# Performance work log

Hardware: AMD Instinct MI355X
Metric: run time of the kernel (lower is better)

## Reference

```python
import jax, jax.numpy as jnp
import numpy as np

B, DIM, H, W = 16, 512, 32, 32
N_CB, VOCAB, D_CB = 8, 1024, 64  # DIM == N_CB * D_CB


def setup_inputs() -> dict:
    key = jax.random.key(0)
    k1, k2 = jax.random.split(key)
    z = jax.random.normal(k1, (B, DIM, H, W), dtype=jnp.float32)
    codebooks = jax.random.normal(k2, (N_CB, VOCAB, D_CB), dtype=jnp.float32) * 0.02
    return {"z": z, "codebooks": codebooks}


def reference(z, codebooks):
    # Eval-mode forward of the multi-codebook (residual-style) VQ:
    # per-codebook squared-distance argmin, gather, straight-through, commitment loss.
    b, d, h, w = z.shape
    n_cb, vocab, d_cb = codebooks.shape
    # rearrange 'b d h w -> (b h w) d', then chunk d into n_cb contiguous parts
    z_flat = z.transpose(0, 2, 3, 1).reshape(-1, n_cb, d_cb)  # (N, n_cb, d_cb)
    # ||z||^2 - 2 z.c + ||c||^2  -> (N, n_cb, vocab)
    dists = (
        jnp.sum(z_flat * z_flat, axis=-1, keepdims=True)
        - 2.0 * jnp.einsum("ncd,cvd->ncv", z_flat, codebooks)
        + jnp.sum(codebooks * codebooks, axis=-1)[None, :, :]
    )
    idx = jnp.argmin(dists, axis=-1)  # (N, n_cb) int
    # gather per-codebook nearest embedding
    q = codebooks[jnp.arange(n_cb)[None, :], idx]  # (N, n_cb, d_cb)
    # commitment: mean over all elements (equal-size chunks => same as per-chunk mse averaged)
    commitment = jnp.mean((z_flat - jax.lax.stop_gradient(q)) ** 2)
    # straight-through estimator
    q_st = z_flat + jax.lax.stop_gradient(q - z_flat)
    quantized = q_st.reshape(b, h, w, d).transpose(0, 3, 1, 2)  # (B, D, H, W)
    indices = idx.reshape(b, h, w, n_cb).transpose(0, 3, 1, 2)  # (B, n_cb, H, W)
    return quantized, indices, commitment
```

## Files before the change

kernel.cpp:

```cpp
#include <hip/hip_runtime.h>
#include <float.h>

#define DIM   512
#define HW    1024
#define NCB   8
#define VOC   1024
#define DCB   64

#define THREADS   256
#define POS_TILE  128
#define VCHUNK    128
#define NCHUNK    8
#define CAP       16
#define MARGIN    0.012f

#define Q_ELEMS   8388608
#define I_ELEMS   131072
#define C_OFFSET  8519680

#define WS_CC_OFF 256
#define WS_CB_OFF 33024

typedef __attribute__((ext_vector_type(8))) short          short8;
typedef __attribute__((ext_vector_type(8))) unsigned short ushort8;
typedef __attribute__((ext_vector_type(4))) float          floatx4;

__device__ __forceinline__ unsigned short f2bf(float f) {
    unsigned u = __builtin_bit_cast(unsigned, f);
    unsigned r = u + 0x7FFFu + ((u >> 16) & 1u);
    return (unsigned short)(r >> 16);
}

__global__ __launch_bounds__(128) void vq_prep_kernel(const float* __restrict__ cbk,
                                                      char* __restrict__ ws,
                                                      float* __restrict__ cc,
                                                      unsigned short* __restrict__ cbkBf) {
#pragma clang fp contract(off)
    int t = blockIdx.x * 128 + threadIdx.x;
    if (t == 0) { ((float*)ws)[0] = 0.f; ((unsigned*)ws)[1] = 0u; }
    const float4* row = (const float4*)(cbk + (long)t * DCB);
    float c[64];
#pragma unroll
    for (int i = 0; i < 16; ++i) {
        float4 v = row[i];
        c[i * 4 + 0] = v.x; c[i * 4 + 1] = v.y;
        c[i * 4 + 2] = v.z; c[i * 4 + 3] = v.w;
    }
    float r[8];
#pragma unroll
    for (int j = 0; j < 8; ++j) { float sq = c[j] * c[j]; r[j] = sq; }
#pragma unroll
    for (int i = 1; i < 8; ++i)
#pragma unroll
        for (int j = 0; j < 8; ++j) { float sq = c[i * 8 + j] * c[i * 8 + j]; r[j] = r[j] + sq; }
    cc[t] = ((r[0] + r[1]) + (r[2] + r[3])) + ((r[4] + r[5]) + (r[6] + r[7]));
    const int swz = (t & 7) << 3;
#pragma unroll
    for (int g8 = 0; g8 < 8; ++g8) {
        ushort8 w;
#pragma unroll
        for (int e = 0; e < 8; ++e) w[e] = f2bf(-2.0f * c[g8 * 8 + e]);
        *(ushort8*)&cbkBf[(long)t * 64 + ((g8 * 8) ^ swz)] = w;
    }
}

struct SmemT {
    unsigned short zsb[POS_TILE * DCB];
    unsigned short csb[2][VCHUNK * DCB];
    float          ccS[VOC];
    unsigned       candI[POS_TILE * CAP];
    unsigned       cnt[POS_TILE];
    unsigned       idxF[POS_TILE];
    float          wred[4];
};

__device__ __forceinline__ void stage_cb(unsigned short* ldsDst,
                                         const unsigned short* gSrc,
                                         int wid, int lane) {
#pragma unroll
    for (int i = 0; i < 4; ++i) {
        const int off = wid * 2048 + i * 512;
        const unsigned short* g = gSrc + off + lane * 8;
        unsigned short* l = ldsDst + off;
        __builtin_amdgcn_global_load_lds(
            (const __attribute__((address_space(1))) unsigned int*)(const void*)g,
            (__attribute__((address_space(3))) unsigned int*)(void*)l,
            16, 0, 0);
    }
}

__device__ __forceinline__ float np_dist_stream(const float* zcol, const float4* cr,
                                                float zz, float ccv) {
#pragma clang fp contract(off)
    float p[16];
#pragma unroll
    for (int l = 0; l < 16; ++l) p[l] = 0.f;
#pragma unroll
    for (int j = 0; j < 4; ++j) {
        float4 c0 = cr[j * 4 + 0], c1 = cr[j * 4 + 1];
        float4 c2 = cr[j * 4 + 2], c3 = cr[j * 4 + 3];
        float cl[16] = {c0.x, c0.y, c0.z, c0.w, c1.x, c1.y, c1.z, c1.w,
                        c2.x, c2.y, c2.z, c2.w, c3.x, c3.y, c3.z, c3.w};
#pragma unroll
        for (int l = 0; l < 16; ++l)
            p[l] = __builtin_fmaf(zcol[(long)(j * 16 + l) * POS_TILE], cl[l], p[l]);
    }
    float s8[8], s4[4];
#pragma unroll
    for (int l = 0; l < 8; ++l) s8[l] = p[l] + p[l + 8];
#pragma unroll
    for (int l = 0; l < 4; ++l) s4[l] = s8[l] + s8[l + 4];
    float u0 = s4[0] + s4[2];
    float u1 = s4[1] + s4[3];
    float E  = u0 + u1;
    float t  = zz - 2.0f * E;
    return t + ccv;
}

__global__ __launch_bounds__(THREADS, 2) void vq_main_kernel(
    const float* __restrict__ z, const float* __restrict__ cbk,
    const float* __restrict__ ccTab, const unsigned short* __restrict__ cbkBf,
    float* __restrict__ commitWs, unsigned* __restrict__ doneCnt,
    float* __restrict__ out)
{
    __shared__ SmemT sm;

    const int tid   = threadIdx.x;
    const int lane  = tid & 63;
    const int wid   = tid >> 6;
    const int l15   = lane & 15;
    const int lg    = lane >> 4;
    const int wpos0 = wid * 32;
    const int cb    = blockIdx.x & 7;
    const int tile  = blockIdx.x >> 3;
    const int b     = tile >> 3;
    const int hw0   = (tile & 7) * POS_TILE;

    const long zBase  = (long)b * (DIM * HW) + (long)cb * DCB * HW + hw0;
    const long cbBase = (long)cb * (VOC * DCB);
    const unsigned short* cbkBfCb = cbkBf + cbBase;

    stage_cb(sm.csb[0], cbkBfCb, wid, lane);

    for (int i = 0; i < 16; ++i) {
        int e   = i * THREADS + tid;
        int kp  = e >> 7;
        int pos = e & 127;
        int k   = kp * 2;
        float v0 = z[zBase + (long)k * HW + pos];
        float v1 = z[zBase + (long)(k + 1) * HW + pos];
        unsigned pack = (unsigned)f2bf(v0) | ((unsigned)f2bf(v1) << 16);
        *(unsigned*)&sm.zsb[pos * 64 + (k ^ ((pos & 7) << 3))] = pack;
    }
    ((float4*)sm.ccS)[tid] = ((const float4*)(ccTab + cb * VOC))[tid];
    if (tid < POS_TILE) sm.cnt[tid] = 0;
    __syncthreads();

    float runBest[2] = {FLT_MAX, FLT_MAX};
    int cur = 0;

    for (int chunk = 0; chunk < NCHUNK; ++chunk) {
        if (chunk < 7)
            stage_cb(sm.csb[cur ^ 1], cbkBfCb + (long)(chunk + 1) * VCHUNK * DCB, wid, lane);

        const unsigned short* cs = sm.csb[cur];

        floatx4 acc[8][2];
#pragma unroll
        for (int ct = 0; ct < 8; ++ct) {
            float4 ci = *(const float4*)&sm.ccS[chunk * VCHUNK + ct * 16 + lg * 4];
            floatx4 a = {ci.x, ci.y, ci.z, ci.w};
            acc[ct][0] = a; acc[ct][1] = a;
        }

#pragma unroll
        for (int ks = 0; ks < 2; ++ks) {
            short8 bz[2];
#pragma unroll
            for (int pt = 0; pt < 2; ++pt) {
                int row = wpos0 + pt * 16 + l15;
                bz[pt] = *(const short8*)&sm.zsb[row * 64 + ((ks * 32 + lg * 8) ^ ((row & 7) << 3))];
            }
#pragma unroll
            for (int ct = 0; ct < 8; ++ct) {
                int crow = ct * 16 + l15;
                short8 ac = *(const short8*)&cs[crow * 64 + ((ks * 32 + lg * 8) ^ ((crow & 7) << 3))];
#pragma unroll
                for (int pt = 0; pt < 2; ++pt)
                    acc[ct][pt] = __builtin_amdgcn_mfma_f32_16x16x32_bf16(ac, bz[pt], acc[ct][pt], 0, 0, 0);
            }
        }

#pragma unroll
        for (int pt = 0; pt < 2; ++pt) {
            float m = acc[0][pt][0];
#pragma unroll
            for (int ct = 0; ct < 8; ++ct)
#pragma unroll
                for (int r = 0; r < 4; ++r) m = fminf(m, acc[ct][pt][r]);
            m = fminf(m, __shfl_xor(m, 16, 64));
            m = fminf(m, __shfl_xor(m, 32, 64));
            runBest[pt] = fminf(runBest[pt], m);
            const float thr = runBest[pt] + MARGIN;
            const int pos = wpos0 + pt * 16 + l15;
#pragma unroll
            for (int ct = 0; ct < 8; ++ct)
#pragma unroll
                for (int r = 0; r < 4; ++r) {
                    if (acc[ct][pt][r] <= thr) {
                        unsigned idx  = chunk * VCHUNK + ct * 16 + lg * 4 + r;
                        unsigned slot = atomicAdd(&sm.cnt[pos], 1u);
                        if (slot < CAP) sm.candI[pos * CAP + slot] = idx;
                    }
                }
        }
        __syncthreads();
        cur ^= 1;
    }

    float* zf32 = (float*)sm.csb;
#pragma unroll
    for (int i = 0; i < 8; ++i) {
        int e4   = i * THREADS + tid;
        int k    = e4 >> 5;
        int posq = e4 & 31;
        float4 v = *(const float4*)(z + zBase + (long)k * HW + posq * 4);
        *(float4*)&zf32[k * POS_TILE + posq * 4] = v;
    }
    __syncthreads();

    if (tid < POS_TILE) {
        const int pos = tid;
        const float* zcol = zf32 + pos;
        float zz;
        {
#pragma clang fp contract(off)
            float r[8];
#pragma unroll
            for (int j = 0; j < 8; ++j) { float v = zcol[(long)j * POS_TILE]; r[j] = v * v; }
#pragma unroll
            for (int i = 1; i < 8; ++i)
#pragma unroll
                for (int j = 0; j < 8; ++j) {
                    float v = zcol[(long)(i * 8 + j) * POS_TILE];
                    r[j] = r[j] + v * v;
                }
            zz = ((r[0] + r[1]) + (r[2] + r[3])) + ((r[4] + r[5]) + (r[6] + r[7]));
        }
        const unsigned n = sm.cnt[pos];
        float bd = FLT_MAX; unsigned bi = 0xFFFFFFFFu;
        if (n <= CAP) {
            for (unsigned s = 0; s < n; ++s) {
                unsigned vi = sm.candI[pos * CAP + s];
                float d = np_dist_stream(zcol, (const float4*)(cbk + cbBase + (long)vi * DCB),
                                         zz, sm.ccS[vi]);
                if (d < bd || (d == bd && vi < bi)) { bd = d; bi = vi; }
            }
        } else {
            for (unsigned vi = 0; vi < VOC; ++vi) {
                float d = np_dist_stream(zcol, (const float4*)(cbk + cbBase + (long)vi * DCB),
                                         zz, sm.ccS[vi]);
                if (d < bd) { bd = d; bi = vi; }
            }
        }
        sm.idxF[pos] = bi;
        out[Q_ELEMS + (long)b * (NCB * HW) + cb * HW + hw0 + pos] = (float)bi;
    }
    __syncthreads();

    {
        const int pos   = tid & 127;
        const int khalf = tid >> 7;
        const unsigned vi = sm.idxF[pos];
        const float* crow = cbk + cbBase + (long)vi * DCB + khalf * 32;
        const float* zcol = zf32 + pos + khalf * 32 * POS_TILE;
        float* qp = out + (long)b * (DIM * HW) + (long)(cb * DCB + khalf * 32) * HW + hw0 + pos;
        float csum = 0.f;
#pragma unroll
        for (int j4 = 0; j4 < 8; ++j4) {
            float4 cv = *(const float4*)(crow + j4 * 4);
            float z0 = zcol[(j4 * 4 + 0) * POS_TILE];
            float z1 = zcol[(j4 * 4 + 1) * POS_TILE];
            float z2 = zcol[(j4 * 4 + 2) * POS_TILE];
            float z3 = zcol[(j4 * 4 + 3) * POS_TILE];
            qp[(long)(j4 * 4 + 0) * HW] = (cv.x - z0) + z0;
            qp[(long)(j4 * 4 + 1) * HW] = (cv.y - z1) + z1;
            qp[(long)(j4 * 4 + 2) * HW] = (cv.z - z2) + z2;
            qp[(long)(j4 * 4 + 3) * HW] = (cv.w - z3) + z3;
            float d0 = z0 - cv.x; csum = fmaf(d0, d0, csum);
            float d1 = z1 - cv.y; csum = fmaf(d1, d1, csum);
            float d2 = z2 - cv.z; csum = fmaf(d2, d2, csum);
            float d3 = z3 - cv.w; csum = fmaf(d3, d3, csum);
        }
#pragma unroll
        for (int m = 1; m < 64; m <<= 1) csum += __shfl_xor(csum, m, 64);
        if (lane == 0) sm.wred[wid] = csum;
    }
    __syncthreads();

    if (tid == 0) {
        atomicAdd(commitWs, sm.wred[0] + sm.wred[1] + sm.wred[2] + sm.wred[3]);
        __threadfence();
        unsigned d = atomicAdd(doneCnt, 1u);
        if (d == 1023u) {
            __threadfence();
            float tot = atomicAdd(commitWs, 0.0f);
            out[C_OFFSET] = tot * (1.0f / 8388608.0f);
        }
    }
}

extern "C" void kernel_launch(void* const* d_in, const int* in_sizes, int n_in,
                              void* d_out, int out_size, void* d_ws, size_t ws_size,
                              hipStream_t stream) {
    (void)in_sizes; (void)n_in; (void)out_size; (void)ws_size;
    const float* z   = (const float*)d_in[0];
    const float* cbk = (const float*)d_in[1];
    float* out = (float*)d_out;
    char*  ws  = (char*)d_ws;
    float*          commitWs = (float*)ws;
    unsigned*       doneCnt  = (unsigned*)(ws + 4);
    float*          ccTab    = (float*)(ws + WS_CC_OFF);
    unsigned short* cbkBf    = (unsigned short*)(ws + WS_CB_OFF);

    vq_prep_kernel<<<dim3(64), dim3(128), 0, stream>>>(cbk, ws, ccTab, cbkBf);
    vq_main_kernel<<<dim3(1024), dim3(THREADS), 0, stream>>>(z, cbk, ccTab, cbkBf,
                                                             commitWs, doneCnt, out);
}
```

Measured before the change: 193.4 us.

## Pre-swizzle codebook into MFMA fragment layout and read directly from global

The prep kernel now writes the bf16 codebook already arranged in per-lane MFMA operand order, so the main kernel loads A fragments straight from global/L2 instead of double-buffering chunks through LDS with barriers. The z fragments are held in registers for all chunks, the fp32 z tile and cc table are no longer staged in LDS, and the rescoring and quantize steps run per wave from global memory with a shuffle instead of block barriers. The smaller LDS footprint allows a launch bound of four blocks per SM, and the commitment sum is spread over 64 atomic slots. The cost is more global/L2 traffic and latency per MFMA operand load, with no LDS reuse across waves.

```diff
diff --git a/kernel.cpp b/kernel.cpp
--- a/kernel.cpp
+++ b/kernel.cpp
@@ -18,8 +18,10 @@
 #define I_ELEMS   131072
 #define C_OFFSET  8519680
 
-#define WS_CC_OFF 256
-#define WS_CB_OFF 33024
+#define WS_DONE_OFF   0
+#define WS_SLOT_OFF   256
+#define WS_CC_OFF     1024
+#define WS_CB_OFF     33792
 
 typedef __attribute__((ext_vector_type(8))) short          short8;
 typedef __attribute__((ext_vector_type(8))) unsigned short ushort8;
@@ -31,66 +33,64 @@
     return (unsigned short)(r >> 16);
 }
 
-__global__ __launch_bounds__(128) void vq_prep_kernel(const float* __restrict__ cbk,
-                                                      char* __restrict__ ws,
+__global__ __launch_bounds__(256) void vq_prep_kernel(const float* __restrict__ cbk,
+                                                      unsigned* __restrict__ doneCnt,
+                                                      float* __restrict__ slots,
                                                       float* __restrict__ cc,
                                                       unsigned short* __restrict__ cbkBf) {
 #pragma clang fp contract(off)
-    int t = blockIdx.x * 128 + threadIdx.x;
-    if (t == 0) { ((float*)ws)[0] = 0.f; ((unsigned*)ws)[1] = 0u; }
-    const float4* row = (const float4*)(cbk + (long)t * DCB);
-    float c[64];
-#pragma unroll
+    __shared__ float zr[256 * 65];
+    const int tid   = threadIdx.x;
+    const int rows0 = blockIdx.x * 256;
+
+    if (blockIdx.x == 0 && tid < 65) {
+        if (tid == 0) *doneCnt = 0u;
+        else slots[tid - 1] = 0.f;
+    }
+
     for (int i = 0; i < 16; ++i) {
-        float4 v = row[i];
-        c[i * 4 + 0] = v.x; c[i * 4 + 1] = v.y;
-        c[i * 4 + 2] = v.z; c[i * 4 + 3] = v.w;
-    }
-    float r[8];
-#pragma unroll
-    for (int j = 0; j < 8; ++j) { float sq = c[j] * c[j]; r[j] = sq; }
-#pragma unroll
-    for (int i = 1; i < 8; ++i)
-#pragma unroll
-        for (int j = 0; j < 8; ++j) { float sq = c[i * 8 + j] * c[i * 8 + j]; r[j] = r[j] + sq; }
-    cc[t] = ((r[0] + r[1]) + (r[2] + r[3])) + ((r[4] + r[5]) + (r[6] + r[7]));
-    const int swz = (t & 7) << 3;
-#pragma unroll
-    for (int g8 = 0; g8 < 8; ++g8) {
+        int e4  = i * 256 + tid;
+        int row = e4 >> 4;
+        int k4  = (e4 & 15) * 4;
+        float4 v = ((const float4*)cbk)[(long)rows0 * 16 + e4];
+        zr[row * 65 + k4 + 0] = v.x;
+        zr[row * 65 + k4 + 1] = v.y;
+        zr[row * 65 + k4 + 2] = v.z;
+        zr[row * 65 + k4 + 3] = v.w;
+    }
+    __syncthreads();
+
+    {
+        const float* c = &zr[tid * 65];
+        float r[8];
+#pragma unroll
+        for (int j = 0; j < 8; ++j) { float v = c[j]; r[j] = v * v; }
+#pragma unroll
+        for (int i = 1; i < 8; ++i)
+#pragma unroll
+            for (int j = 0; j < 8; ++j) { float v = c[i * 8 + j]; r[j] = r[j] + v * v; }
+        cc[rows0 + tid] = ((r[0] + r[1]) + (r[2] + r[3])) + ((r[4] + r[5]) + (r[6] + r[7]));
+    }
+
+#pragma unroll
+    for (int it = 0; it < 8; ++it) {
+        int row = it * 32 + (tid >> 3);
+        int g8  = tid & 7;
         ushort8 w;
 #pragma unroll
-        for (int e = 0; e < 8; ++e) w[e] = f2bf(-2.0f * c[g8 * 8 + e]);
-        *(ushort8*)&cbkBf[(long)t * 64 + ((g8 * 8) ^ swz)] = w;
-    }
-}
-
-struct SmemT {
-    unsigned short zsb[POS_TILE * DCB];
-    unsigned short csb[2][VCHUNK * DCB];
-    float          ccS[VOC];
-    unsigned       candI[POS_TILE * CAP];
-    unsigned       cnt[POS_TILE];
-    unsigned       idxF[POS_TILE];
-    float          wred[4];
-};
-
-__device__ __forceinline__ void stage_cb(unsigned short* ldsDst,
-                                         const unsigned short* gSrc,
-                                         int wid, int lane) {
-#pragma unroll
-    for (int i = 0; i < 4; ++i) {
-        const int off = wid * 2048 + i * 512;
-        const unsigned short* g = gSrc + off + lane * 8;
-        unsigned short* l = ldsDst + off;
-        __builtin_amdgcn_global_load_lds(
-            (const __attribute__((address_space(1))) unsigned int*)(const void*)g,
-            (__attribute__((address_space(3))) unsigned int*)(void*)l,
-            16, 0, 0);
-    }
-}
-
-__device__ __forceinline__ float np_dist_stream(const float* zcol, const float4* cr,
-                                                float zz, float ccv) {
+        for (int e = 0; e < 8; ++e) w[e] = f2bf(-2.0f * zr[row * 65 + g8 * 8 + e]);
+        int g     = rows0 + row;
+        int code  = g & 1023;
+        int chunk = code >> 7, ct = (code >> 4) & 7, l15 = code & 15;
+        int ks    = g8 >> 2,  lg = g8 & 3;
+        long dst = (long)(g >> 10) * 65536 +
+                   ((((chunk * 8 + ct) * 2 + ks) * 64) + lg * 16 + l15) * 8;
+        *(ushort8*)&cbkBf[dst] = w;
+    }
+}
+
+__device__ __forceinline__ float np_dist_g(const float* zp, const float4* cr,
+                                           float zz, float ccv) {
 #pragma clang fp contract(off)
     float p[16];
 #pragma unroll
@@ -103,7 +103,7 @@
                         c2.x, c2.y, c2.z, c2.w, c3.x, c3.y, c3.z, c3.w};
 #pragma unroll
         for (int l = 0; l < 16; ++l)
-            p[l] = __builtin_fmaf(zcol[(long)(j * 16 + l) * POS_TILE], cl[l], p[l]);
+            p[l] = __builtin_fmaf(zp[(long)(j * 16 + l) * HW], cl[l], p[l]);
     }
     float s8[8], s4[4];
 #pragma unroll
@@ -117,10 +117,16 @@
     return t + ccv;
 }
 
-__global__ __launch_bounds__(THREADS, 2) void vq_main_kernel(
+struct SmemT {
+    unsigned short zsb[POS_TILE * DCB];
+    unsigned       candI[POS_TILE * CAP];
+    unsigned       cnt[POS_TILE];
+};
+
+__global__ __launch_bounds__(THREADS, 4) void vq_main_kernel(
     const float* __restrict__ z, const float* __restrict__ cbk,
     const float* __restrict__ ccTab, const unsigned short* __restrict__ cbkBf,
-    float* __restrict__ commitWs, unsigned* __restrict__ doneCnt,
+    float* __restrict__ slots, unsigned* __restrict__ doneCnt,
     float* __restrict__ out)
 {
     __shared__ SmemT sm;
@@ -138,9 +144,8 @@
 
     const long zBase  = (long)b * (DIM * HW) + (long)cb * DCB * HW + hw0;
     const long cbBase = (long)cb * (VOC * DCB);
-    const unsigned short* cbkBfCb = cbkBf + cbBase;
-
-    stage_cb(sm.csb[0], cbkBfCb, wid, lane);
+    const unsigned short* cbA  = cbkBf + (long)cb * 65536;
+    const float*          ccRow = ccTab + cb * VOC;
 
     for (int i = 0; i < 16; ++i) {
         int e   = i * THREADS + tid;
@@ -152,44 +157,37 @@
         unsigned pack = (unsigned)f2bf(v0) | ((unsigned)f2bf(v1) << 16);
         *(unsigned*)&sm.zsb[pos * 64 + (k ^ ((pos & 7) << 3))] = pack;
     }
-    ((float4*)sm.ccS)[tid] = ((const float4*)(ccTab + cb * VOC))[tid];
     if (tid < POS_TILE) sm.cnt[tid] = 0;
     __syncthreads();
 
+    short8 bz[2][2];
+#pragma unroll
+    for (int pt = 0; pt < 2; ++pt)
+#pragma unroll
+        for (int ks = 0; ks < 2; ++ks) {
+            int row = wpos0 + pt * 16 + l15;
+            bz[pt][ks] = *(const short8*)&sm.zsb[row * 64 + ((ks * 32 + lg * 8) ^ ((row & 7) << 3))];
+        }
+
     float runBest[2] = {FLT_MAX, FLT_MAX};
-    int cur = 0;
 
     for (int chunk = 0; chunk < NCHUNK; ++chunk) {
-        if (chunk < 7)
-            stage_cb(sm.csb[cur ^ 1], cbkBfCb + (long)(chunk + 1) * VCHUNK * DCB, wid, lane);
-
-        const unsigned short* cs = sm.csb[cur];
-
         floatx4 acc[8][2];
 #pragma unroll
         for (int ct = 0; ct < 8; ++ct) {
-            float4 ci = *(const float4*)&sm.ccS[chunk * VCHUNK + ct * 16 + lg * 4];
+            float4 ci = *(const float4*)&ccRow[chunk * VCHUNK + ct * 16 + lg * 4];
             floatx4 a = {ci.x, ci.y, ci.z, ci.w};
             acc[ct][0] = a; acc[ct][1] = a;
         }
-
-#pragma unroll
-        for (int ks = 0; ks < 2; ++ks) {
-            short8 bz[2];
-#pragma unroll
-            for (int pt = 0; pt < 2; ++pt) {
-                int row = wpos0 + pt * 16 + l15;
-                bz[pt] = *(const short8*)&sm.zsb[row * 64 + ((ks * 32 + lg * 8) ^ ((row & 7) << 3))];
+#pragma unroll
+        for (int ks = 0; ks < 2; ++ks)
+#pragma unroll
+            for (int ct = 0; ct < 8; ++ct) {
+                short8 ac = *(const short8*)&cbA[((((chunk * 8 + ct) * 2 + ks) << 6) + lane) << 3];
+#pragma unroll
+                for (int pt = 0; pt < 2; ++pt)
+                    acc[ct][pt] = __builtin_amdgcn_mfma_f32_16x16x32_bf16(ac, bz[pt][ks], acc[ct][pt], 0, 0, 0);
             }
-#pragma unroll
-            for (int ct = 0; ct < 8; ++ct) {
-                int crow = ct * 16 + l15;
-                short8 ac = *(const short8*)&cs[crow * 64 + ((ks * 32 + lg * 8) ^ ((crow & 7) << 3))];
-#pragma unroll
-                for (int pt = 0; pt < 2; ++pt)
-                    acc[ct][pt] = __builtin_amdgcn_mfma_f32_16x16x32_bf16(ac, bz[pt], acc[ct][pt], 0, 0, 0);
-            }
-        }
 
 #pragma unroll
         for (int pt = 0; pt < 2; ++pt) {
@@ -214,75 +212,62 @@
                     }
                 }
         }
-        __syncthreads();
-        cur ^= 1;
-    }
-
-    float* zf32 = (float*)sm.csb;
-#pragma unroll
-    for (int i = 0; i < 8; ++i) {
-        int e4   = i * THREADS + tid;
-        int k    = e4 >> 5;
-        int posq = e4 & 31;
-        float4 v = *(const float4*)(z + zBase + (long)k * HW + posq * 4);
-        *(float4*)&zf32[k * POS_TILE + posq * 4] = v;
-    }
-    __syncthreads();
-
-    if (tid < POS_TILE) {
-        const int pos = tid;
-        const float* zcol = zf32 + pos;
+    }
+
+    unsigned bi = 0xFFFFFFFFu;
+    if (lane < 32) {
+        const int pos = wpos0 + lane;
+        const float* zp = z + zBase + pos;
         float zz;
         {
 #pragma clang fp contract(off)
             float r[8];
 #pragma unroll
-            for (int j = 0; j < 8; ++j) { float v = zcol[(long)j * POS_TILE]; r[j] = v * v; }
+            for (int j = 0; j < 8; ++j) { float v = zp[(long)j * HW]; r[j] = v * v; }
 #pragma unroll
             for (int i = 1; i < 8; ++i)
 #pragma unroll
                 for (int j = 0; j < 8; ++j) {
-                    float v = zcol[(long)(i * 8 + j) * POS_TILE];
+                    float v = zp[(long)(i * 8 + j) * HW];
                     r[j] = r[j] + v * v;
                 }
             zz = ((r[0] + r[1]) + (r[2] + r[3])) + ((r[4] + r[5]) + (r[6] + r[7]));
         }
         const unsigned n = sm.cnt[pos];
-        float bd = FLT_MAX; unsigned bi = 0xFFFFFFFFu;
+        float bd = FLT_MAX;
         if (n <= CAP) {
             for (unsigned s = 0; s < n; ++s) {
                 unsigned vi = sm.candI[pos * CAP + s];
-                float d = np_dist_stream(zcol, (const float4*)(cbk + cbBase + (long)vi * DCB),
-                                         zz, sm.ccS[vi]);
+                float d = np_dist_g(zp, (const float4*)(cbk + cbBase + (long)vi * DCB),
+                                    zz, ccRow[vi]);
                 if (d < bd || (d == bd && vi < bi)) { bd = d; bi = vi; }
             }
         } else {
             for (unsigned vi = 0; vi < VOC; ++vi) {
-                float d = np_dist_stream(zcol, (const float4*)(cbk + cbBase + (long)vi * DCB),
-                                         zz, sm.ccS[vi]);
+                float d = np_dist_g(zp, (const float4*)(cbk + cbBase + (long)vi * DCB),
+                                    zz, ccRow[vi]);
                 if (d < bd) { bd = d; bi = vi; }
             }
         }
-        sm.idxF[pos] = bi;
         out[Q_ELEMS + (long)b * (NCB * HW) + cb * HW + hw0 + pos] = (float)bi;
     }
-    __syncthreads();
-
+
+    const unsigned vi = (unsigned)__shfl((int)bi, lane & 31, 64);
     {
-        const int pos   = tid & 127;
-        const int khalf = tid >> 7;
-        const unsigned vi = sm.idxF[pos];
+        const int posl  = lane & 31;
+        const int pos   = wpos0 + posl;
+        const int khalf = lane >> 5;
         const float* crow = cbk + cbBase + (long)vi * DCB + khalf * 32;
-        const float* zcol = zf32 + pos + khalf * 32 * POS_TILE;
+        const float* zp   = z + zBase + pos + (long)khalf * 32 * HW;
         float* qp = out + (long)b * (DIM * HW) + (long)(cb * DCB + khalf * 32) * HW + hw0 + pos;
         float csum = 0.f;
 #pragma unroll
         for (int j4 = 0; j4 < 8; ++j4) {
             float4 cv = *(const float4*)(crow + j4 * 4);
-            float z0 = zcol[(j4 * 4 + 0) * POS_TILE];
-            float z1 = zcol[(j4 * 4 + 1) * POS_TILE];
-            float z2 = zcol[(j4 * 4 + 2) * POS_TILE];
-            float z3 = zcol[(j4 * 4 + 3) * POS_TILE];
+            float z0 = zp[(long)(j4 * 4 + 0) * HW];
+            float z1 = zp[(long)(j4 * 4 + 1) * HW];
+            float z2 = zp[(long)(j4 * 4 + 2) * HW];
+            float z3 = zp[(long)(j4 * 4 + 3) * HW];
             qp[(long)(j4 * 4 + 0) * HW] = (cv.x - z0) + z0;
             qp[(long)(j4 * 4 + 1) * HW] = (cv.y - z1) + z1;
             qp[(long)(j4 * 4 + 2) * HW] = (cv.z - z2) + z2;
@@ -294,18 +279,17 @@
         }
 #pragma unroll
         for (int m = 1; m < 64; m <<= 1) csum += __shfl_xor(csum, m, 64);
-        if (lane == 0) sm.wred[wid] = csum;
-    }
-    __syncthreads();
-
-    if (tid == 0) {
-        atomicAdd(commitWs, sm.wred[0] + sm.wred[1] + sm.wred[2] + sm.wred[3]);
-        __threadfence();
-        unsigned d = atomicAdd(doneCnt, 1u);
-        if (d == 1023u) {
+
+        if (lane == 0) {
+            atomicAdd(&slots[(blockIdx.x * 4 + wid) & 63], csum);
             __threadfence();
-            float tot = atomicAdd(commitWs, 0.0f);
-            out[C_OFFSET] = tot * (1.0f / 8388608.0f);
+            unsigned d = atomicAdd(doneCnt, 1u);
+            if (d == 4095u) {
+                __threadfence();
+                float tot = 0.f;
+                for (int s = 0; s < 64; ++s) tot += slots[s];
+                out[C_OFFSET] = tot * (1.0f / 8388608.0f);
+            }
         }
     }
 }
@@ -318,12 +302,12 @@
     const float* cbk = (const float*)d_in[1];
     float* out = (float*)d_out;
     char*  ws  = (char*)d_ws;
-    float*          commitWs = (float*)ws;
-    unsigned*       doneCnt  = (unsigned*)(ws + 4);
-    float*          ccTab    = (float*)(ws + WS_CC_OFF);
-    unsigned short* cbkBf    = (unsigned short*)(ws + WS_CB_OFF);
-
-    vq_prep_kernel<<<dim3(64), dim3(128), 0, stream>>>(cbk, ws, ccTab, cbkBf);
+    unsigned*       doneCnt = (unsigned*)(ws + WS_DONE_OFF);
+    float*          slots   = (float*)(ws + WS_SLOT_OFF);
+    float*          ccTab   = (float*)(ws + WS_CC_OFF);
+    unsigned short* cbkBf   = (unsigned short*)(ws + WS_CB_OFF);
+
+    vq_prep_kernel<<<dim3(32), dim3(256), 0, stream>>>(cbk, doneCnt, slots, ccTab, cbkBf);
     vq_main_kernel<<<dim3(1024), dim3(THREADS), 0, stream>>>(z, cbk, ccTab, cbkBf,
-                                                             commitWs, doneCnt, out);
-}
+                                                             slots, doneCnt, out);
+}
```

After: 287.6 us. 1.49x slower.
